# Kernel optimization log

Measured on AMD Instinct MI355X. Metric: run time of the kernel, lower is better.

The kernel has to match this reference:

```python
import jax, jax.numpy as jnp
import numpy as np

EPS = 1e-5
H, W, D_FULL, D_RFFT, DIM = 9, 11, 9, 5, 900  # spectral grid 9x11x9, rfft last dim -> 5

def layer_norm(x, gamma, beta):
    mu = jnp.mean(x, axis=-1, keepdims=True)
    var = jnp.var(x, axis=-1, keepdims=True)
    return (x - mu) * jax.lax.rsqrt(var + EPS) * gamma + beta

def setup_inputs() -> dict:
    key = jax.random.key(0)
    ks = jax.random.split(key, 12)
    B, N, C = 64, H * W * D_FULL, DIM  # N = 891
    hidden, rank = int(C * 2.0), C // 2  # 1800, 450
    return {
        "x": jax.random.normal(ks[0], (B, N, C), dtype=jnp.float32),
        # Global_Filter complex weight: (h, w, d, dim, 2), init ~ N(0,1)*0.02
        "cw": jax.random.normal(ks[1], (H, W, D_RFFT, C, 2), dtype=jnp.float32) * 0.02,
        "gamma1": jnp.ones((C,), jnp.float32),
        "beta1": jnp.zeros((C,), jnp.float32),
        "gamma2": jnp.ones((C,), jnp.float32),
        "beta2": jnp.zeros((C,), jnp.float32),
        # low-rank MLP (torch Linear weights are (out, in); we apply x @ W.T)
        "u1_w": jax.random.normal(ks[2], (rank, C), jnp.float32) * (1.0 / np.sqrt(C)),
        "v1_w": jax.random.normal(ks[3], (hidden, rank), jnp.float32) * (1.0 / np.sqrt(rank)),
        "v1_b": jnp.zeros((hidden,), jnp.float32),
        "u2_w": jax.random.normal(ks[4], (rank, hidden), jnp.float32) * (1.0 / np.sqrt(hidden)),
        "v2_w": jax.random.normal(ks[5], (C, rank), jnp.float32) * (1.0 / np.sqrt(rank)),
        "v2_b": jnp.zeros((C,), jnp.float32),
    }

def reference(x, cw, gamma1, beta1, gamma2, beta2, u1_w, v1_w, v1_b, u2_w, v2_w, v2_b):
    B, N, C = x.shape
    # norm1 -> global spectral filter
    y = layer_norm(x, gamma1, beta1)
    y = y.reshape(B, H, W, D_FULL, C)
    yf = jnp.fft.rfftn(y, axes=(1, 2, 3), norm="ortho")  # (B, 9, 11, 5, C) complex
    weight = jax.lax.complex(cw[..., 0], cw[..., 1])      # (9, 11, 5, C)
    yf = yf * weight
    y = jnp.fft.irfftn(yf, s=(H, W, D_FULL), axes=(1, 2, 3), norm="ortho")
    y = y.reshape(B, N, C)
    # norm2 -> low-rank MLP (dropout/droppath = identity in eval)
    z = layer_norm(y, gamma2, beta2)
    z = jnp.einsum("bnc,rc->bnr", z, u1_w)
    z = jnp.einsum("bnr,hr->bnh", z, v1_w) + v1_b
    z = jax.nn.gelu(z, approximate=False)
    z = jnp.einsum("bnh,rh->bnr", z, u2_w)
    z = jnp.einsum("bnr,cr->bnc", z, v2_w) + v2_b
    return x + z
```

## Files before the change

### kernel.cpp

```cpp
#include <hip/hip_runtime.h>


typedef unsigned short u16;
typedef __bf16 bf16x8 __attribute__((ext_vector_type(8)));
typedef float f32x4 __attribute__((ext_vector_type(4)));

#define LN_EPS 1e-5f
#define CH 16

constexpr float KC9[9] = {
  1.0f, 0.766044443118978f, 0.17364817766693041f, -0.4999999999999998f,
  -0.9396926207859083f, -0.9396926207859084f, -0.5000000000000004f,
  0.17364817766692997f, 0.7660444431189778f };
constexpr float KS9[9] = {
  0.0f, 0.6427876096865393f, 0.984807753012208f, 0.8660254037844387f,
  0.3420201433256689f, -0.34202014332566866f, -0.8660254037844385f,
  -0.9848077530122081f, -0.6427876096865396f };
constexpr float KC11[11] = {
  1.0f, 0.8412535328311812f, 0.41541501300188644f, -0.14231483827328512f,
  -0.654860733945285f, -0.9594929736144974f, -0.9594929736144974f,
  -0.6548607339452852f, -0.14231483827328543f, 0.4154150130018863f,
  0.8412535328311811f };
constexpr float KS11[11] = {
  0.0f, 0.5406408174555976f, 0.9096319953545183f, 0.9898214418809327f,
  0.7557495743542583f, 0.2817325568414297f, -0.2817325568414296f,
  -0.7557495743542582f, -0.9898214418809327f, -0.9096319953545184f,
  -0.5406408174555979f };

__device__ __forceinline__ u16 f2bf(float f) {
  unsigned int u = __float_as_uint(f);
  return (u16)((u + 0x7fffu + ((u >> 16) & 1u)) >> 16);
}
__device__ __forceinline__ float gelu_f(float v) {
  float t = 0.7978845608028654f * v * (1.f + 0.044715f * v * v);
  float e = __expf(2.f * t);
  float th = 1.f - 2.f * __builtin_amdgcn_rcpf(e + 1.f);
  return 0.5f * v * (1.f + th);
}

__global__ __launch_bounds__(256) void k_cvt(const float* __restrict__ s, u16* __restrict__ d,
                                             int rows, int sc, int dc,
                                             const float* __restrict__ gamma) {
  int i = blockIdx.x * 256 + threadIdx.x;
  if (i >= rows * dc) return;
  int r = i / dc, c = i % dc;
  u16 o = 0;
  if (c < sc) {
    float v = s[(size_t)r * sc + c];
    if (gamma) v *= gamma[c];
    o = f2bf(v);
  }
  d[i] = o;
}

__global__ __launch_bounds__(256) void k_bias1(const float* __restrict__ u1w,
                                               const float* __restrict__ b2,
                                               float* __restrict__ out) {
  int r = blockIdx.x * 256 + threadIdx.x;
  if (r < 450) {
    float s = 0.f;
    for (int c = 0; c < 900; c++) s += u1w[r * 900 + c] * b2[c];
    out[r] = s;
  }
}

__global__ __launch_bounds__(256) void k_stats1(const float* __restrict__ x,
                                                float2* __restrict__ stats) {
  int tok = blockIdx.x * 4 + (threadIdx.x >> 6);
  int l = threadIdx.x & 63;
  const float* row = x + (size_t)tok * 900;
  float s1 = 0.f, s2 = 0.f;
#pragma unroll
  for (int j = 0; j < 15; j++) {
    int c = l + j * 64;
    if (c < 900) { float a = row[c]; s1 += a; s2 += a * a; }
  }
#pragma unroll
  for (int off = 32; off; off >>= 1) { s1 += __shfl_xor(s1, off, 64); s2 += __shfl_xor(s2, off, 64); }
  if (l == 0) {
    float m = s1 * (1.f / 900.f);
    float var = s2 * (1.f / 900.f) - m * m;
    stats[tok] = make_float2(m, rsqrtf(var + LN_EPS));
  }
}

__global__ __launch_bounds__(256) void k_spectral(const float* __restrict__ x,
                                                  const float2* __restrict__ stats,
                                                  const float* __restrict__ g1,
                                                  const float* __restrict__ b1,
                                                  const float* __restrict__ cw,
                                                  float* __restrict__ y) {
  __shared__ float sre[5 * 99 * CH];
  __shared__ float sim[5 * 99 * CH];
  int b = blockIdx.x / 57, cc = blockIdx.x % 57;
  int c0 = cc * CH;
  int t = threadIdx.x;
  const float* xb = x + (size_t)b * 801900;
  const float2* st = stats + (size_t)b * 891;

  for (int col = t; col < 99 * CH; col += 256) {
    int pos = col / CH, c = col % CH;
    int cg = c0 + c; bool ok = cg < 900;
    float g = ok ? g1[cg] : 0.f, be = ok ? b1[cg] : 0.f;
    float yv[9];
#pragma unroll
    for (int d = 0; d < 9; d++) {
      float a = ok ? xb[(size_t)(pos * 9 + d) * 900 + cg] : 0.f;
      float2 s = st[pos * 9 + d];
      yv[d] = (a - s.x) * s.y * g + be;
    }
#pragma unroll
    for (int kd = 0; kd < 5; kd++) {
      float re = 0.f, im = 0.f;
#pragma unroll
      for (int d = 0; d < 9; d++) { int j = (kd * d) % 9; re += yv[d] * KC9[j]; im -= yv[d] * KS9[j]; }
      sre[(kd * 99 + pos) * CH + c] = re;
      sim[(kd * 99 + pos) * CH + c] = im;
    }
  }
  __syncthreads();

  for (int col = t; col < 5 * 9 * CH; col += 256) {
    int kd = col / (9 * CH), r = col % (9 * CH), h = r / CH, c = r % CH;
    int base = (kd * 99 + h * 11) * CH + c;
    float xr[11], xi[11];
#pragma unroll
    for (int w = 0; w < 11; w++) { xr[w] = sre[base + w * CH]; xi[w] = sim[base + w * CH]; }
#pragma unroll
    for (int k = 0; k < 11; k++) {
      float yr = 0.f, yi = 0.f;
#pragma unroll
      for (int w = 0; w < 11; w++) {
        int j = (k * w) % 11; float cf = KC11[j], sf = KS11[j];
        yr += xr[w] * cf + xi[w] * sf;
        yi += xi[w] * cf - xr[w] * sf;
      }
      sre[base + k * CH] = yr; sim[base + k * CH] = yi;
    }
  }
  __syncthreads();

  for (int col = t; col < 5 * 11 * CH; col += 256) {
    int kd = col / (11 * CH), r = col % (11 * CH), kw = r / CH, c = r % CH;
    int cg = c0 + c;
    int base = (kd * 99 + kw) * CH + c;
    float xr[9], xi[9];
#pragma unroll
    for (int h = 0; h < 9; h++) { xr[h] = sre[base + h * 11 * CH]; xi[h] = sim[base + h * 11 * CH]; }
    float zr[9], zi[9];
#pragma unroll
    for (int k = 0; k < 9; k++) {
      float yr = 0.f, yi = 0.f;
#pragma unroll
      for (int h = 0; h < 9; h++) {
        int j = (k * h) % 9; float cf = KC9[j], sf = KS9[j];
        yr += xr[h] * cf + xi[h] * sf;
        yi += xi[h] * cf - xr[h] * sf;
      }
      float wr = 0.f, wi = 0.f;
      if (cg < 900) {
        size_t widx = ((size_t)((k * 11 + kw) * 5 + kd) * 900 + cg) * 2;
        wr = cw[widx]; wi = cw[widx + 1];
      }
      zr[k] = yr * wr - yi * wi;
      zi[k] = yr * wi + yi * wr;
    }
#pragma unroll
    for (int h = 0; h < 9; h++) {
      float orr = 0.f, oi = 0.f;
#pragma unroll
      for (int k = 0; k < 9; k++) {
        int j = (k * h) % 9; float cf = KC9[j], sf = KS9[j];
        orr += zr[k] * cf - zi[k] * sf;
        oi  += zi[k] * cf + zr[k] * sf;
      }
      sre[base + h * 11 * CH] = orr; sim[base + h * 11 * CH] = oi;
    }
  }
  __syncthreads();

  for (int col = t; col < 5 * 9 * CH; col += 256) {
    int kd = col / (9 * CH), r = col % (9 * CH), h = r / CH, c = r % CH;
    int base = (kd * 99 + h * 11) * CH + c;
    float xr[11], xi[11];
#pragma unroll
    for (int w = 0; w < 11; w++) { xr[w] = sre[base + w * CH]; xi[w] = sim[base + w * CH]; }
#pragma unroll
    for (int k = 0; k < 11; k++) {
      float yr = 0.f, yi = 0.f;
#pragma unroll
      for (int w = 0; w < 11; w++) {
        int j = (k * w) % 11; float cf = KC11[j], sf = KS11[j];
        yr += xr[w] * cf - xi[w] * sf;
        yi += xi[w] * cf + xr[w] * sf;
      }
      sre[base + k * CH] = yr; sim[base + k * CH] = yi;
    }
  }
  __syncthreads();

  for (int col = t; col < 99 * CH; col += 256) {
    int pos = col / CH, c = col % CH;
    int cg = c0 + c;
    if (cg >= 900) continue;
    float Xr[5], Xi[5];
#pragma unroll
    for (int k = 0; k < 5; k++) { Xr[k] = sre[(k * 99 + pos) * CH + c]; Xi[k] = sim[(k * 99 + pos) * CH + c]; }
#pragma unroll
    for (int d = 0; d < 9; d++) {
      float acc = Xr[0];
#pragma unroll
      for (int k = 1; k < 5; k++) { int j = (k * d) % 9; acc += 2.f * (Xr[k] * KC9[j] - Xi[k] * KS9[j]); }
      y[((size_t)b * 891 + pos * 9 + d) * 900 + cg] = acc * (1.f / 891.f);
    }
  }
}

__global__ __launch_bounds__(256) void k_ln2(const float* __restrict__ y, u16* __restrict__ yn) {
  int tok = blockIdx.x * 4 + (threadIdx.x >> 6);
  int l = threadIdx.x & 63;
  const float* row = y + (size_t)tok * 900;
  float v[15];
  float s1 = 0.f, s2 = 0.f;
#pragma unroll
  for (int j = 0; j < 15; j++) {
    int c = l + j * 64;
    float a = (c < 900) ? row[c] : 0.f;
    v[j] = a; s1 += a; s2 += a * a;
  }
#pragma unroll
  for (int off = 32; off; off >>= 1) { s1 += __shfl_xor(s1, off, 64); s2 += __shfl_xor(s2, off, 64); }
  float m = s1 * (1.f / 900.f);
  float var = s2 * (1.f / 900.f) - m * m;
  float rs = rsqrtf(var + LN_EPS);
  u16* orow = yn + (size_t)tok * 928;
#pragma unroll
  for (int j = 0; j < 15; j++) {
    int c = l + j * 64;
    if (c < 900) orow[c] = f2bf((v[j] - m) * rs);
    else if (c < 928) orow[c] = 0;
  }
}

typedef __attribute__((address_space(1))) void gvoid;
typedef __attribute__((address_space(3))) void svoid;

__device__ __forceinline__ void stage16(const u16* g, u16* lbase) {
  __builtin_amdgcn_global_load_lds((gvoid*)(void*)g, (svoid*)lbase, 16, 0, 0);
}

__device__ __forceinline__ void stage_tile(const u16* __restrict__ A, const u16* __restrict__ B,
                                           int m0, int n0, int M, int N, int ldk, int k0,
                                           u16* As, u16* Bs, int w, int l) {
  int arow = (w << 4) + (l >> 2);
  int koff = k0 + (((l & 3) ^ ((l >> 3) & 3)) << 3);
#pragma unroll
  for (int j = 0; j < 2; j++) {
    int r = (j << 6) + arow;
    int gm = m0 + r; gm = gm < M ? gm : M - 1;
    stage16(A + (size_t)gm * ldk + koff, &As[((j << 6) + (w << 4)) * 32]);
    int gn = n0 + r; gn = gn < N ? gn : N - 1;
    stage16(B + (size_t)gn * ldk + koff, &Bs[((j << 6) + (w << 4)) * 32]);
  }
}

template <int EPI>
__global__ __launch_bounds__(256, 2) void k_gemm(
    const u16* __restrict__ A, const u16* __restrict__ B,
    int M, int N, int Kt, int ldk, int NT,
    u16* __restrict__ Ob, int ldo, int Nstore,
    const float* __restrict__ bias,
    const float* __restrict__ Xres, float* __restrict__ Of) {
  __shared__ u16 As[2][128 * 32];
  __shared__ u16 Bs[2][128 * 32];
  int t = threadIdx.x, w = t >> 6, l = t & 63;
  int mt = blockIdx.x / NT, nt = blockIdx.x % NT;
  int m0 = mt * 128, n0 = nt * 128;
  int wm = (w >> 1) << 6, wn = (w & 1) << 6;
  int fr = l & 15, fq = l >> 4;
  int rsw = ((fq ^ ((fr >> 1) & 3)) << 3);

  f32x4 acc[4][4];
  f32x4 zero = {0.f, 0.f, 0.f, 0.f};
#pragma unroll
  for (int i = 0; i < 4; i++)
#pragma unroll
    for (int j = 0; j < 4; j++) acc[i][j] = zero;

  stage_tile(A, B, m0, n0, M, N, ldk, 0, As[0], Bs[0], w, l);
  if (Kt > 1) stage_tile(A, B, m0, n0, M, N, ldk, 32, As[1], Bs[1], w, l);

  for (int kt = 0; kt < Kt; ++kt) {
    if (kt + 1 < Kt) asm volatile("s_waitcnt vmcnt(4)\n\ts_barrier" ::: "memory");
    else             asm volatile("s_waitcnt vmcnt(0)\n\ts_barrier" ::: "memory");

    const u16* as = As[kt & 1];
    const u16* bs = Bs[kt & 1];
    bf16x8 af[4], bfr[4];
#pragma unroll
    for (int i = 0; i < 4; i++) af[i] = *(const bf16x8*)&as[(wm + (i << 4) + fr) * 32 + rsw];
#pragma unroll
    for (int i = 0; i < 4; i++) bfr[i] = *(const bf16x8*)&bs[(wn + (i << 4) + fr) * 32 + rsw];
#pragma unroll
    for (int i = 0; i < 4; i++)
#pragma unroll
      for (int j = 0; j < 4; j++)
        acc[i][j] = __builtin_amdgcn_mfma_f32_16x16x32_bf16(af[i], bfr[j], acc[i][j], 0, 0, 0);

    asm volatile("s_barrier" ::: "memory");
    if (kt + 2 < Kt)
      stage_tile(A, B, m0, n0, M, N, ldk, (kt + 2) * 32, As[kt & 1], Bs[kt & 1], w, l);
  }

#pragma unroll
  for (int j = 0; j < 4; j++) {
    int gn = n0 + wn + (j << 4) + fr;
    float bv = 0.f;
    if (EPI != 2) bv = (gn < Nstore) ? bias[gn] : 0.f;
#pragma unroll
    for (int i = 0; i < 4; i++) {
#pragma unroll
      for (int r = 0; r < 4; r++) {
        int gm = m0 + wm + (i << 4) + (fq << 2) + r;
        if (gm < M) {
          float val = acc[i][j][r] + bv;
          if (EPI == 1) val = gelu_f(val);
          if (EPI == 3) {
            if (gn < Nstore) Of[(size_t)gm * Nstore + gn] = val + Xres[(size_t)gm * Nstore + gn];
          } else {
            if (gn < ldo) Ob[(size_t)gm * ldo + gn] = (gn < Nstore) ? f2bf(val) : (u16)0;
          }
        }
      }
    }
  }
}

extern "C" void kernel_launch(void* const* d_in, const int* in_sizes, int n_in,
                              void* d_out, int out_size, void* d_ws, size_t ws_size,
                              hipStream_t stream) {
  const float* x   = (const float*)d_in[0];
  const float* cw  = (const float*)d_in[1];
  const float* g1  = (const float*)d_in[2];
  const float* b1  = (const float*)d_in[3];
  const float* g2  = (const float*)d_in[4];
  const float* b2  = (const float*)d_in[5];
  const float* u1w = (const float*)d_in[6];
  const float* v1w = (const float*)d_in[7];
  const float* v1b = (const float*)d_in[8];
  const float* u2w = (const float*)d_in[9];
  const float* v2w = (const float*)d_in[10];
  const float* v2b = (const float*)d_in[11];

  char* ws = (char*)d_ws;
  float* y   = (float*)ws;
  u16*   t2  = (u16*)ws;
  u16*   t3  = (u16*)(ws + 228096000);
  u16*   u1g = (u16*)(ws + 286488576);
  u16*   v1c = (u16*)(ws + 287323776);
  u16*   u2c = (u16*)(ws + 289166976);
  u16*   v2c = (u16*)(ws + 290808576);
  float* b1r = (float*)(ws + 291730176);

  u16*    yn    = (u16*)d_out;
  u16*    t1    = (u16*)((char*)d_out + 105836544);
  float2* stats = (float2*)((char*)d_out + 164229120);
  float*  outF  = (float*)d_out;

  k_cvt<<<1632, 256, 0, stream>>>(u1w, u1g, 450, 900, 928, g2);
  k_cvt<<<3600, 256, 0, stream>>>(v1w, v1c, 1800, 450, 512, nullptr);
  k_cvt<<<3207, 256, 0, stream>>>(u2w, u2c, 450, 1800, 1824, nullptr);
  k_cvt<<<1800, 256, 0, stream>>>(v2w, v2c, 900, 450, 512, nullptr);
  k_bias1<<<2, 256, 0, stream>>>(u1w, b2, b1r);

  k_stats1<<<14256, 256, 0, stream>>>(x, stats);
  k_spectral<<<64 * 57, 256, 0, stream>>>(x, stats, g1, b1, cw, y);
  k_ln2<<<14256, 256, 0, stream>>>(y, yn);

  k_gemm<0><<<446 * 4,  256, 0, stream>>>(yn, u1g, 57024, 450,  29, 928,  4,  t1, 512, 450, b1r, nullptr, nullptr);
  k_gemm<1><<<446 * 15, 256, 0, stream>>>(t1, v1c, 57024, 1800, 16, 512,  15, t2, 1824, 1800, v1b, nullptr, nullptr);
  k_gemm<2><<<446 * 4,  256, 0, stream>>>(t2, u2c, 57024, 450,  57, 1824, 4,  t3, 512, 450, nullptr, nullptr, nullptr);
  k_gemm<3><<<446 * 8,  256, 0, stream>>>(t3, v2c, 57024, 900,  16, 512,  8,  nullptr, 0, 900, v2b, x, outF);
}
```

Before: 1.494 ms.

## Enlarge GEMM tiles to 256x256x64 with 512-thread blocks

Reworks the bf16 MFMA GEMM from 128x128 tiles with K-step 32 and 4 waves to 256x256 tiles with K-step 64 and 8 waves. Each wave now computes a 128x64 sub-tile, using a new 8-way XOR LDS swizzle and s_setprio around the MFMA bursts. K-padding for the intermediate buffers grows to multiples of 64, and the workspace offsets and conversion launches are updated to match. The aim is more data reuse per global and LDS load and fewer blocks. In exchange the kernel uses 128KB of LDS per block and more accumulator registers, which may cap occupancy, and the large tiles waste work on the N=450 GEMMs.

New measurement: 1.735 ms. 1.16x slower.

```diff
diff --git a/kernel.cpp b/kernel.cpp
--- a/kernel.cpp
+++ b/kernel.cpp
@@ -233,12 +233,12 @@
   float m = s1 * (1.f / 900.f);
   float var = s2 * (1.f / 900.f) - m * m;
   float rs = rsqrtf(var + LN_EPS);
-  u16* orow = yn + (size_t)tok * 928;
+  u16* orow = yn + (size_t)tok * 960;
 #pragma unroll
   for (int j = 0; j < 15; j++) {
     int c = l + j * 64;
     if (c < 900) orow[c] = f2bf((v[j] - m) * rs);
-    else if (c < 928) orow[c] = 0;
+    else orow[c] = 0;
   }
 }
 
@@ -251,65 +251,71 @@
 
 __device__ __forceinline__ void stage_tile(const u16* __restrict__ A, const u16* __restrict__ B,
                                            int m0, int n0, int M, int N, int ldk, int k0,
-                                           u16* As, u16* Bs, int w, int l) {
-  int arow = (w << 4) + (l >> 2);
-  int koff = k0 + (((l & 3) ^ ((l >> 3) & 3)) << 3);
-#pragma unroll
-  for (int j = 0; j < 2; j++) {
-    int r = (j << 6) + arow;
+                                           u16* As, u16* Bs, int t) {
+#pragma unroll
+  for (int j = 0; j < 4; j++) {
+    int g = (j << 9) + t;
+    int r = g >> 3;
+    int cs = ((g & 7) ^ (r & 7)) << 3;
     int gm = m0 + r; gm = gm < M ? gm : M - 1;
-    stage16(A + (size_t)gm * ldk + koff, &As[((j << 6) + (w << 4)) * 32]);
+    stage16(A + (size_t)gm * ldk + k0 + cs, &As[g << 3]);
     int gn = n0 + r; gn = gn < N ? gn : N - 1;
-    stage16(B + (size_t)gn * ldk + koff, &Bs[((j << 6) + (w << 4)) * 32]);
+    stage16(B + (size_t)gn * ldk + k0 + cs, &Bs[g << 3]);
   }
 }
 
 template <int EPI>
-__global__ __launch_bounds__(256, 2) void k_gemm(
+__global__ __launch_bounds__(512, 2) void k_gemm(
     const u16* __restrict__ A, const u16* __restrict__ B,
     int M, int N, int Kt, int ldk, int NT,
     u16* __restrict__ Ob, int ldo, int Nstore,
     const float* __restrict__ bias,
     const float* __restrict__ Xres, float* __restrict__ Of) {
-  __shared__ u16 As[2][128 * 32];
-  __shared__ u16 Bs[2][128 * 32];
+  __shared__ __align__(16) u16 As[2][256 * 64];
+  __shared__ __align__(16) u16 Bs[2][256 * 64];
   int t = threadIdx.x, w = t >> 6, l = t & 63;
   int mt = blockIdx.x / NT, nt = blockIdx.x % NT;
-  int m0 = mt * 128, n0 = nt * 128;
-  int wm = (w >> 1) << 6, wn = (w & 1) << 6;
+  int m0 = mt << 8, n0 = nt << 8;
+  int wm = (w >> 2) << 7;
+  int wn = (w & 3) << 6;
   int fr = l & 15, fq = l >> 4;
-  int rsw = ((fq ^ ((fr >> 1) & 3)) << 3);
-
-  f32x4 acc[4][4];
+
+  f32x4 acc[8][4];
   f32x4 zero = {0.f, 0.f, 0.f, 0.f};
 #pragma unroll
-  for (int i = 0; i < 4; i++)
+  for (int i = 0; i < 8; i++)
 #pragma unroll
     for (int j = 0; j < 4; j++) acc[i][j] = zero;
 
-  stage_tile(A, B, m0, n0, M, N, ldk, 0, As[0], Bs[0], w, l);
-  if (Kt > 1) stage_tile(A, B, m0, n0, M, N, ldk, 32, As[1], Bs[1], w, l);
+  stage_tile(A, B, m0, n0, M, N, ldk, 0, As[0], Bs[0], t);
+  if (Kt > 1) stage_tile(A, B, m0, n0, M, N, ldk, 64, As[1], Bs[1], t);
 
   for (int kt = 0; kt < Kt; ++kt) {
-    if (kt + 1 < Kt) asm volatile("s_waitcnt vmcnt(4)\n\ts_barrier" ::: "memory");
+    if (kt + 1 < Kt) asm volatile("s_waitcnt vmcnt(8)\n\ts_barrier" ::: "memory");
     else             asm volatile("s_waitcnt vmcnt(0)\n\ts_barrier" ::: "memory");
 
     const u16* as = As[kt & 1];
     const u16* bs = Bs[kt & 1];
-    bf16x8 af[4], bfr[4];
-#pragma unroll
-    for (int i = 0; i < 4; i++) af[i] = *(const bf16x8*)&as[(wm + (i << 4) + fr) * 32 + rsw];
-#pragma unroll
-    for (int i = 0; i < 4; i++) bfr[i] = *(const bf16x8*)&bs[(wn + (i << 4) + fr) * 32 + rsw];
-#pragma unroll
-    for (int i = 0; i < 4; i++)
-#pragma unroll
-      for (int j = 0; j < 4; j++)
-        acc[i][j] = __builtin_amdgcn_mfma_f32_16x16x32_bf16(af[i], bfr[j], acc[i][j], 0, 0, 0);
+#pragma unroll
+    for (int ks = 0; ks < 2; ks++) {
+      int csw = ((((ks << 2) | fq) ^ (fr & 7)) << 3);
+      bf16x8 af[8], bfv[4];
+#pragma unroll
+      for (int i = 0; i < 8; i++) af[i] = *(const bf16x8*)&as[(wm + (i << 4) + fr) * 64 + csw];
+#pragma unroll
+      for (int j = 0; j < 4; j++) bfv[j] = *(const bf16x8*)&bs[(wn + (j << 4) + fr) * 64 + csw];
+      __builtin_amdgcn_s_setprio(1);
+#pragma unroll
+      for (int i = 0; i < 8; i++)
+#pragma unroll
+        for (int j = 0; j < 4; j++)
+          acc[i][j] = __builtin_amdgcn_mfma_f32_16x16x32_bf16(af[i], bfv[j], acc[i][j], 0, 0, 0);
+      __builtin_amdgcn_s_setprio(0);
+    }
 
     asm volatile("s_barrier" ::: "memory");
     if (kt + 2 < Kt)
-      stage_tile(A, B, m0, n0, M, N, ldk, (kt + 2) * 32, As[kt & 1], Bs[kt & 1], w, l);
+      stage_tile(A, B, m0, n0, M, N, ldk, (kt + 2) << 6, As[kt & 1], Bs[kt & 1], t);
   }
 
 #pragma unroll
@@ -318,7 +324,7 @@
     float bv = 0.f;
     if (EPI != 2) bv = (gn < Nstore) ? bias[gn] : 0.f;
 #pragma unroll
-    for (int i = 0; i < 4; i++) {
+    for (int i = 0; i < 8; i++) {
 #pragma unroll
       for (int r = 0; r < 4; r++) {
         int gm = m0 + wm + (i << 4) + (fq << 2) + r;
@@ -355,21 +361,21 @@
   char* ws = (char*)d_ws;
   float* y   = (float*)ws;
   u16*   t2  = (u16*)ws;
-  u16*   t3  = (u16*)(ws + 228096000);
-  u16*   u1g = (u16*)(ws + 286488576);
-  u16*   v1c = (u16*)(ws + 287323776);
-  u16*   u2c = (u16*)(ws + 289166976);
-  u16*   v2c = (u16*)(ws + 290808576);
-  float* b1r = (float*)(ws + 291730176);
+  u16*   t3  = (u16*)(ws + 211673088);
+  u16*   u1g = (u16*)(ws + 270065664);
+  u16*   v1c = (u16*)(ws + 270929664);
+  u16*   u2c = (u16*)(ws + 272772864);
+  u16*   v2c = (u16*)(ws + 274443264);
+  float* b1r = (float*)(ws + 275364864);
 
   u16*    yn    = (u16*)d_out;
-  u16*    t1    = (u16*)((char*)d_out + 105836544);
-  float2* stats = (float2*)((char*)d_out + 164229120);
+  u16*    t1    = (u16*)((char*)d_out + 109486080);
+  float2* stats = (float2*)((char*)d_out + 167878656);
   float*  outF  = (float*)d_out;
 
-  k_cvt<<<1632, 256, 0, stream>>>(u1w, u1g, 450, 900, 928, g2);
+  k_cvt<<<1688, 256, 0, stream>>>(u1w, u1g, 450, 900, 960, g2);
   k_cvt<<<3600, 256, 0, stream>>>(v1w, v1c, 1800, 450, 512, nullptr);
-  k_cvt<<<3207, 256, 0, stream>>>(u2w, u2c, 450, 1800, 1824, nullptr);
+  k_cvt<<<3263, 256, 0, stream>>>(u2w, u2c, 450, 1800, 1856, nullptr);
   k_cvt<<<1800, 256, 0, stream>>>(v2w, v2c, 900, 450, 512, nullptr);
   k_bias1<<<2, 256, 0, stream>>>(u1w, b2, b1r);
 
@@ -377,8 +383,8 @@
   k_spectral<<<64 * 57, 256, 0, stream>>>(x, stats, g1, b1, cw, y);
   k_ln2<<<14256, 256, 0, stream>>>(y, yn);
 
-  k_gemm<0><<<446 * 4,  256, 0, stream>>>(yn, u1g, 57024, 450,  29, 928,  4,  t1, 512, 450, b1r, nullptr, nullptr);
-  k_gemm<1><<<446 * 15, 256, 0, stream>>>(t1, v1c, 57024, 1800, 16, 512,  15, t2, 1824, 1800, v1b, nullptr, nullptr);
-  k_gemm<2><<<446 * 4,  256, 0, stream>>>(t2, u2c, 57024, 450,  57, 1824, 4,  t3, 512, 450, nullptr, nullptr, nullptr);
-  k_gemm<3><<<446 * 8,  256, 0, stream>>>(t3, v2c, 57024, 900,  16, 512,  8,  nullptr, 0, 900, v2b, x, outF);
-}
+  k_gemm<0><<<223 * 2, 512, 0, stream>>>(yn, u1g, 57024, 450,  15, 960,  2, t1, 512, 450, b1r, nullptr, nullptr);
+  k_gemm<1><<<223 * 8, 512, 0, stream>>>(t1, v1c, 57024, 1800, 8,  512,  8, t2, 1856, 1800, v1b, nullptr, nullptr);
+  k_gemm<2><<<223 * 2, 512, 0, stream>>>(t2, u2c, 57024, 450,  29, 1856, 2, t3, 512, 450, nullptr, nullptr, nullptr);
+  k_gemm<3><<<223 * 4, 512, 0, stream>>>(t3, v2c, 57024, 900,  8,  512,  4, nullptr, 0, 900, v2b, x, outF);
+}
```
